# Optimization experiments

Hardware: AMD Instinct MI355X
Metric: run time of the kernel (lower is better)

Reference implementation:

```python
import jax, jax.numpy as jnp
import numpy as np

DN = ('NCDHW', 'OIDHW', 'NCDHW')
EPS = 1e-5


def conv3(x, w, b):
    y = jax.lax.conv_general_dilated(x, w, (1, 1, 1), 'SAME', dimension_numbers=DN)
    return y + b[None, :, None, None, None]


def inorm(x):
    # InstanceNorm3d, affine=False: normalize over spatial dims per (batch, channel)
    m = jnp.mean(x, axis=(2, 3, 4), keepdims=True)
    v = jnp.mean((x - m) ** 2, axis=(2, 3, 4), keepdims=True)
    return (x - m) * jax.lax.rsqrt(v + EPS)


def prelu(x, a):
    return jnp.where(x >= 0, x, a * x)


def _head(x, w1, b1, w234, b234, a, wf, bf, K):
    # 4-conv tower (conv + instancenorm + PReLU), then final conv -> (b, n_anchors_level, K)
    x = prelu(inorm(conv3(x, w1, b1)), a[0])
    for i in range(3):
        x = prelu(inorm(conv3(x, w234[i], b234[i])), a[i + 1])
    y = conv3(x, wf, bf)
    y = jnp.transpose(y, (0, 2, 3, 4, 1))  # (b, D, H, W, C)
    return y.reshape(y.shape[0], -1, K)


def setup_inputs() -> dict:
    key = jax.random.key(0)
    ks = jax.random.split(key, 32)
    IN_C, FEAT = 36, 64
    CLS_OUT = 9 * 2      # out_channels_per_pos * headers
    REG_OUT = 9 * 3 * 2  # out_channels_per_pos * dim * 2
    inp = {}
    shapes = [(1, IN_C, 32, 32, 32), (1, IN_C, 16, 16, 16), (1, IN_C, 8, 8, 8), (1, IN_C, 4, 4, 4)]
    for i, s in enumerate(shapes):
        inp[f'p{i}'] = jax.random.normal(ks[i], s, dtype=jnp.float32)
    w = lambda k, s: jax.random.normal(k, s, dtype=jnp.float32) * 0.05
    for j, h in enumerate(['cls', 'reg']):
        base = 4 + j * 10
        OUT = CLS_OUT if h == 'cls' else REG_OUT
        inp[f'{h}_w1'] = w(ks[base + 0], (FEAT, IN_C, 3, 3, 3))
        inp[f'{h}_b1'] = jnp.zeros((FEAT,), jnp.float32)
        inp[f'{h}_w234'] = w(ks[base + 1], (3, FEAT, FEAT, 3, 3, 3))
        inp[f'{h}_b234'] = jnp.zeros((3, FEAT), jnp.float32)
        inp[f'{h}_a'] = jnp.full((4,), 0.25, jnp.float32)  # PReLU init
        inp[f'{h}_wf'] = w(ks[base + 2], (OUT, FEAT, 3, 3, 3))
        inp[f'{h}_bf'] = jnp.zeros((OUT,), jnp.float32)
    return inp


def reference(p0, p1, p2, p3,
              cls_w1, cls_b1, cls_w234, cls_b234, cls_a, cls_wf, cls_bf,
              reg_w1, reg_b1, reg_w234, reg_b234, reg_a, reg_wf, reg_bf):
    feats = [p0, p1, p2, p3]
    class_logits = jnp.concatenate(
        [_head(p, cls_w1, cls_b1, cls_w234, cls_b234, cls_a, cls_wf, cls_bf, 2) for p in feats], axis=1)
    bb_outputs = jnp.concatenate(
        [_head(p, reg_w1, reg_b1, reg_w234, reg_b234, reg_a, reg_wf, reg_bf, 6) for p in feats], axis=1)
    return class_logits, bb_outputs
```

## Files before the change

kernel.cpp:

```cpp
#include <hip/hip_runtime.h>


typedef __attribute__((ext_vector_type(8)))  short short8;
typedef __attribute__((ext_vector_type(8)))  unsigned short ushort8;
typedef __attribute__((ext_vector_type(4)))  float f32x4;

static constexpr int TOTVOX    = 37440;
static constexpr int CLS_TOTAL = 673920;
static constexpr int TOTPADV   = 46352;
static constexpr size_t PAD_HSTRIDE_E = (size_t)TOTPADV * 64;
static constexpr size_t WLAYER_E = 2u * 27 * 4096;

__device__ __forceinline__ unsigned short f2b(float x) {
    unsigned int u = __float_as_uint(x);
    u += 0x7FFFu + ((u >> 16) & 1u);
    return (unsigned short)(u >> 16);
}
__device__ __forceinline__ float b2f(unsigned short h) {
    return __uint_as_float(((unsigned)h) << 16);
}

__device__ __forceinline__ int xcdswz(int orig) {
    const int xcd = orig & 7;
    return (xcd < 2 ? xcd * 147 : 294 + (xcd - 2) * 146) + (orig >> 3);
}

__device__ __forceinline__ void blkdec(int b, int& lvl, int& ls, int& S, int& P,
                                       int& loff, int& cvol, int& base)
{
    if (b < 1024)      { lvl = 0; base = b * 32; }
    else if (b < 1152) { lvl = 1; base = 32768 + (b - 1024) * 32; }
    else if (b < 1168) { lvl = 2; base = 36864 + (b - 1152) * 32; }
    else               { lvl = 3; base = 37376 + (b - 1168) * 32; }
    ls = 5 - lvl; S = 1 << ls; P = S + 2;
    loff = (lvl == 0) ? 0 : (lvl == 1) ? 32768 : (lvl == 2) ? 36864 : 37376;
    cvol = (lvl == 0) ? 0 : (lvl == 1) ? 39304 : (lvl == 2) ? 45136 : 46136;
}

__device__ __forceinline__ void voxdec(int vox, int& lvl, int& ls, int& loff,
                                       int& cvol, int& pbase)
{
    if (vox < 32768)      lvl = 0;
    else if (vox < 36864) lvl = 1;
    else if (vox < 37376) lvl = 2;
    else                  lvl = 3;
    ls = 5 - lvl;
    const int S = 1 << ls, P = S + 2;
    loff = (lvl == 0) ? 0 : (lvl == 1) ? 32768 : (lvl == 2) ? 36864 : 37376;
    cvol = (lvl == 0) ? 0 : (lvl == 1) ? 39304 : (lvl == 2) ? 45136 : 46136;
    const int v = vox - loff;
    const int x = v & (S - 1), y = (v >> ls) & (S - 1), z = v >> (2 * ls);
    pbase = ((z + 1) * P + (y + 1)) * P + (x + 1);
}

__global__ __launch_bounds__(256) void wconv_kernel(
    const float* __restrict__ cls_w1, const float* __restrict__ reg_w1,
    const float* __restrict__ cls_w234, const float* __restrict__ reg_w234,
    const float* __restrict__ cls_wf, const float* __restrict__ reg_wf,
    unsigned short* __restrict__ dst)
{
    const int id = blockIdx.x * 256 + (int)threadIdx.x;
    const int s  = id / 221184;
    const int r  = id - s * 221184;
    const int head = r / 110592;
    const int r2 = r - head * 110592;
    const int t  = r2 >> 12;
    const int q  = r2 & 4095;
    const int slice = q >> 9;
    const int co = (q >> 3) & 63;
    const int ci = slice * 8 + (q & 7);

    float val = 0.0f;
    if (s == 0) {
        if (ci < 36) {
            const float* w = head ? reg_w1 : cls_w1;
            val = w[(co * 36 + ci) * 27 + t];
        }
    } else if (s <= 3) {
        const float* w = (head ? reg_w234 : cls_w234) + (size_t)(s - 1) * 110592;
        val = w[(co * 64 + ci) * 27 + t];
    } else {
        const int OUT = head ? 54 : 18;
        if (co < OUT) {
            const float* w = head ? reg_wf : cls_wf;
            val = w[(co * 64 + ci) * 27 + t];
        }
    }
    dst[id] = f2b(val);
}

__global__ __launch_bounds__(256) void inconv_kernel(
    const float* __restrict__ p0, const float* __restrict__ p1,
    const float* __restrict__ p2, const float* __restrict__ p3,
    unsigned short* __restrict__ padin)
{
    const int id = blockIdx.x * 256 + (int)threadIdx.x;
    const int s   = id / 37440;
    const int vox = id - s * 37440;

    int lvl, ls, loff, cvol, pbase;
    voxdec(vox, lvl, ls, loff, cvol, pbase);
    const int nvox = 1 << (3 * ls);
    const int lvox = vox - loff;
    const float* src = (lvl == 0) ? p0 : (lvl == 1) ? p1 : (lvl == 2) ? p2 : p3;

    ushort8 o;
    #pragma unroll
    for (int j = 0; j < 8; ++j) {
        const int c = s * 8 + j;
        o[j] = (c < 36) ? f2b(src[c * nvox + lvox]) : (unsigned short)0;
    }
    *reinterpret_cast<ushort8*>(padin + ((size_t)s * TOTPADV + cvol + pbase) * 8) = o;
}

template<bool FINAL>
__global__ __launch_bounds__(256, 4) void conv_mfma_kernel(
    const unsigned short* __restrict__ A, const size_t a_head_stride_e,
    const unsigned short* __restrict__ W,
    const float* __restrict__ b_cls, const float* __restrict__ b_reg,
    float* __restrict__ stats, unsigned short* __restrict__ raw,
    float* __restrict__ dout)
{
    const int tid  = threadIdx.x;
    const int head = blockIdx.y;
    const int b    = xcdswz(blockIdx.x);

    int lvl, ls, S, P, loff, cvol, base;
    blkdec(b, lvl, ls, S, P, loff, cvol, base);

    const int lane = tid & 63, wv = tid >> 6;
    const int row = lane & 15, kg = lane >> 4;
    const int cout = wv * 16 + row;

    const unsigned short* Abase = A + (size_t)head * a_head_stride_e;
    const unsigned short* Wh = W + (size_t)head * (27 * 4096);

    unsigned av00, av01, av10, av11, wv0, wv1;
    {
        const int v0 = (base - loff) + row;
        const int x0 = v0 & (S - 1), y0 = (v0 >> ls) & (S - 1), z0 = v0 >> (2 * ls);
        const int pb0 = ((z0 + 1) * P + (y0 + 1)) * P + (x0 + 1);
        const int v1 = (base - loff) + 16 + row;
        const int x1 = v1 & (S - 1), y1 = (v1 >> ls) & (S - 1), z1 = v1 >> (2 * ls);
        const int pb1 = ((z1 + 1) * P + (y1 + 1)) * P + (x1 + 1);
        av00 = (unsigned)(((kg)     * TOTPADV + cvol + pb0) * 16);
        av01 = (unsigned)(((kg + 4) * TOTPADV + cvol + pb0) * 16);
        av10 = (unsigned)(((kg)     * TOTPADV + cvol + pb1) * 16);
        av11 = (unsigned)(((kg + 4) * TOTPADV + cvol + pb1) * 16);
    }
    wv0 = (unsigned)(((kg)     * 64 + cout) * 16);
    wv1 = (unsigned)(((kg + 4) * 64 + cout) * 16);

    f32x4 acc0 = {0.f,0.f,0.f,0.f}, acc1 = acc0;

    short8 a00_0,a01_0,a10_0,a11_0,w0_0,w1_0;
    short8 a00_1,a01_1,a10_1,a11_1,w0_1,w1_1;
    short8 a00_2,a01_2,a10_2,a11_2,w0_2,w1_2;

    auto ISSUE = [&](int t, short8& a00, short8& a01, short8& a10, short8& a11,
                     short8& w0, short8& w1) {
        const int dz = t / 9 - 1, dy = (t / 3) % 3 - 1, dx = t % 3 - 1;
        const unsigned short* At = Abase + (size_t)((dz * P + dy) * P + dx) * 8;
        const unsigned short* Wt = Wh + t * 4096;
        asm volatile("global_load_dwordx4 %0, %1, %2" : "=v"(a00) : "v"(av00), "s"(At));
        asm volatile("global_load_dwordx4 %0, %1, %2" : "=v"(a01) : "v"(av01), "s"(At));
        asm volatile("global_load_dwordx4 %0, %1, %2" : "=v"(a10) : "v"(av10), "s"(At));
        asm volatile("global_load_dwordx4 %0, %1, %2" : "=v"(a11) : "v"(av11), "s"(At));
        asm volatile("global_load_dwordx4 %0, %1, %2" : "=v"(w0)  : "v"(wv0),  "s"(Wt));
        asm volatile("global_load_dwordx4 %0, %1, %2" : "=v"(w1)  : "v"(wv1),  "s"(Wt));
    };
    auto CONS = [&](const short8& a00, const short8& a01, const short8& a10,
                    const short8& a11, const short8& w0, const short8& w1) {
        acc0 = __builtin_amdgcn_mfma_f32_16x16x32_bf16(a00, w0, acc0, 0, 0, 0);
        acc1 = __builtin_amdgcn_mfma_f32_16x16x32_bf16(a10, w0, acc1, 0, 0, 0);
        acc0 = __builtin_amdgcn_mfma_f32_16x16x32_bf16(a01, w1, acc0, 0, 0, 0);
        acc1 = __builtin_amdgcn_mfma_f32_16x16x32_bf16(a11, w1, acc1, 0, 0, 0);
    };

    #define SLOT0 a00_0,a01_0,a10_0,a11_0,w0_0,w1_0
    #define SLOT1 a00_1,a01_1,a10_1,a11_1,w0_1,w1_1
    #define SLOT2 a00_2,a01_2,a10_2,a11_2,w0_2,w1_2
    #define WAITV(N) do { asm volatile("s_waitcnt vmcnt(" #N ")" ::: "memory"); \
                          __builtin_amdgcn_sched_barrier(0); } while (0)

    ISSUE(0, SLOT0); ISSUE(1, SLOT1); ISSUE(2, SLOT2);
    WAITV(12); CONS(SLOT0); ISSUE(3,  SLOT0);
    WAITV(12); CONS(SLOT1); ISSUE(4,  SLOT1);
    WAITV(12); CONS(SLOT2); ISSUE(5,  SLOT2);
    WAITV(12); CONS(SLOT0); ISSUE(6,  SLOT0);
    WAITV(12); CONS(SLOT1); ISSUE(7,  SLOT1);
    WAITV(12); CONS(SLOT2); ISSUE(8,  SLOT2);
    WAITV(12); CONS(SLOT0); ISSUE(9,  SLOT0);
    WAITV(12); CONS(SLOT1); ISSUE(10, SLOT1);
    WAITV(12); CONS(SLOT2); ISSUE(11, SLOT2);
    WAITV(12); CONS(SLOT0); ISSUE(12, SLOT0);
    WAITV(12); CONS(SLOT1); ISSUE(13, SLOT1);
    WAITV(12); CONS(SLOT2); ISSUE(14, SLOT2);
    WAITV(12); CONS(SLOT0); ISSUE(15, SLOT0);
    WAITV(12); CONS(SLOT1); ISSUE(16, SLOT1);
    WAITV(12); CONS(SLOT2); ISSUE(17, SLOT2);
    WAITV(12); CONS(SLOT0); ISSUE(18, SLOT0);
    WAITV(12); CONS(SLOT1); ISSUE(19, SLOT1);
    WAITV(12); CONS(SLOT2); ISSUE(20, SLOT2);
    WAITV(12); CONS(SLOT0); ISSUE(21, SLOT0);
    WAITV(12); CONS(SLOT1); ISSUE(22, SLOT1);
    WAITV(12); CONS(SLOT2); ISSUE(23, SLOT2);
    WAITV(12); CONS(SLOT0); ISSUE(24, SLOT0);
    WAITV(12); CONS(SLOT1); ISSUE(25, SLOT1);
    WAITV(12); CONS(SLOT2); ISSUE(26, SLOT2);
    WAITV(12); CONS(SLOT0);
    WAITV(6);  CONS(SLOT1);
    WAITV(0);  CONS(SLOT2);

    #undef SLOT0
    #undef SLOT1
    #undef SLOT2
    #undef WAITV

    if constexpr (!FINAL) {
        const float bias = (head ? b_reg : b_cls)[cout];
        unsigned short* rp = raw + ((size_t)(head * 8 + (cout >> 3)) * TOTVOX) * 8
                                 + (cout & 7);
        float s1 = 0.f, s2 = 0.f;
        #pragma unroll
        for (int i = 0; i < 2; ++i) {
            const f32x4 a = i ? acc1 : acc0;
            #pragma unroll
            for (int r = 0; r < 4; ++r) {
                const float val = a[r] + bias;
                const int vg = base + i * 16 + kg * 4 + r;
                rp[(size_t)vg * 8] = f2b(val);
                s1 += val; s2 += val * val;
            }
        }
        s1 += __shfl_xor(s1, 16, 64); s1 += __shfl_xor(s1, 32, 64);
        s2 += __shfl_xor(s2, 16, 64); s2 += __shfl_xor(s2, 32, 64);
        if (lane < 16) {
            float* st = stats + ((head * 4 + lvl) * 64 + wv * 16 + lane) * 2;
            atomicAdd(st + 0, s1);
            atomicAdd(st + 1, s2);
        }
    } else {
        const int OUT = head ? 54 : 18;
        if (cout < OUT) {
            const float bias = (head ? b_reg : b_cls)[cout];
            float* ob = dout + (head ? CLS_TOTAL : 0);
            #pragma unroll
            for (int i = 0; i < 2; ++i) {
                const f32x4 a = i ? acc1 : acc0;
                #pragma unroll
                for (int r = 0; r < 4; ++r) {
                    const int vg = base + i * 16 + kg * 4 + r;
                    ob[(size_t)vg * OUT + cout] = a[r] + bias;
                }
            }
        }
    }
}

__global__ __launch_bounds__(256) void norm_kernel(
    const unsigned short* __restrict__ raw, const float* __restrict__ stats,
    const float* __restrict__ a_cls, const float* __restrict__ a_reg,
    const int layer, unsigned short* __restrict__ pad)
{
    const int tid  = threadIdx.x;
    const int head = blockIdx.y;
    const int b    = xcdswz(blockIdx.x);

    int lvl, ls, S, P, loff, cvol, base;
    blkdec(b, lvl, ls, S, P, loff, cvol, base);

    const int vg = base + (tid >> 3);
    const int v  = vg - loff;
    const int s  = tid & 7;
    const int x = v & (S - 1), y = (v >> ls) & (S - 1), z = v >> (2 * ls);
    const int pb = ((z + 1) * P + (y + 1)) * P + (x + 1);

    const float inv_n = 1.0f / (float)(1 << (3 * ls));
    const float alpha = (head ? a_reg : a_cls)[layer];
    const float* st = stats + (size_t)((head * 4 + lvl) * 64) * 2;

    const ushort8 u = *reinterpret_cast<const ushort8*>(
        raw + ((size_t)(head * 8 + s) * TOTVOX + vg) * 8);
    ushort8 o;
    #pragma unroll
    for (int j = 0; j < 8; ++j) {
        const int c = s * 8 + j;
        const float m = st[c * 2] * inv_n;
        float var = st[c * 2 + 1] * inv_n - m * m;
        const float rs = rsqrtf(fmaxf(var, 0.0f) + 1e-5f);
        float val = (b2f(u[j]) - m) * rs;
        val = (val >= 0.0f) ? val : alpha * val;
        o[j] = f2b(val);
    }
    *reinterpret_cast<ushort8*>(pad + (size_t)head * PAD_HSTRIDE_E
                                    + ((size_t)s * TOTPADV + cvol + pb) * 8) = o;
}

extern "C" void kernel_launch(void* const* d_in, const int* in_sizes, int n_in,
                              void* d_out, int out_size, void* d_ws, size_t ws_size,
                              hipStream_t stream)
{
    const float* p0      = (const float*)d_in[0];
    const float* p1      = (const float*)d_in[1];
    const float* p2      = (const float*)d_in[2];
    const float* p3      = (const float*)d_in[3];
    const float* cls_w1  = (const float*)d_in[4];
    const float* cls_b1  = (const float*)d_in[5];
    const float* cls_w234= (const float*)d_in[6];
    const float* cls_b234= (const float*)d_in[7];
    const float* cls_a   = (const float*)d_in[8];
    const float* cls_wf  = (const float*)d_in[9];
    const float* cls_bf  = (const float*)d_in[10];
    const float* reg_w1  = (const float*)d_in[11];
    const float* reg_b1  = (const float*)d_in[12];
    const float* reg_w234= (const float*)d_in[13];
    const float* reg_b234= (const float*)d_in[14];
    const float* reg_a   = (const float*)d_in[15];
    const float* reg_wf  = (const float*)d_in[16];
    const float* reg_bf  = (const float*)d_in[17];

    char* ws = (char*)d_ws;
    float*          stats  = (float*)ws;
    unsigned short* padIn0 = (unsigned short*)(ws + 16384);
    unsigned short* padA   = (unsigned short*)(ws + 5949440);
    unsigned short* padB   = (unsigned short*)(ws + 17815552);
    unsigned short* raw    = (unsigned short*)(ws + 29681664);
    unsigned short* wcvt   = (unsigned short*)(ws + 39266304);

    hipMemsetAsync(ws, 0, 29681664, stream);

    wconv_kernel<<<4320, 256, 0, stream>>>(
        cls_w1, reg_w1, cls_w234, reg_w234, cls_wf, reg_wf, wcvt);
    inconv_kernel<<<1170, 256, 0, stream>>>(p0, p1, p2, p3, padIn0);

    const dim3 cgrid(1170, 2);

    conv_mfma_kernel<false><<<cgrid, 256, 0, stream>>>(
        padIn0, 0, wcvt, cls_b1, reg_b1, stats, raw, nullptr);
    norm_kernel<<<cgrid, 256, 0, stream>>>(raw, stats, cls_a, reg_a, 0, padA);

    unsigned short* srcs[3] = { padA, padB, padA };
    unsigned short* dsts[3] = { padB, padA, padB };
    for (int l = 0; l < 3; ++l) {
        conv_mfma_kernel<false><<<cgrid, 256, 0, stream>>>(
            srcs[l], PAD_HSTRIDE_E, wcvt + (size_t)(l + 1) * WLAYER_E,
            cls_b234 + l * 64, reg_b234 + l * 64,
            stats + (l + 1) * 1024, raw, nullptr);
        norm_kernel<<<cgrid, 256, 0, stream>>>(
            raw, stats + (l + 1) * 1024, cls_a, reg_a, l + 1, dsts[l]);
    }

    conv_mfma_kernel<true><<<cgrid, 256, 0, stream>>>(
        padB, PAD_HSTRIDE_E, wcvt + 4 * WLAYER_E,
        cls_bf, reg_bf, nullptr, nullptr, (float*)d_out);
}
```

Measured before the change: 557.2 us.

## Retile conv MFMA so each wave computes all 64 output channels

Each conv block now covers 128 voxels, and each wave owns 32 voxels across all 64 output channels (4 channel groups) instead of 16 channels. Each activation fragment is loaded once per wave and reused across four weight fragments, cutting redundant activation reads from the padded buffer. The weight layout is permuted to match, the grid shrinks from 1170 to 293 blocks per head, the pipeline goes from three stages to two, and occupancy drops to 3 blocks per SIMD. The costs are more accumulator and operand registers, fewer blocks to fill the GPU, and idle waves on the smallest level.

```diff
diff --git a/kernel.cpp b/kernel.cpp
--- a/kernel.cpp
+++ b/kernel.cpp
@@ -20,13 +20,29 @@
     return __uint_as_float(((unsigned)h) << 16);
 }
 
-__device__ __forceinline__ int xcdswz(int orig) {
+__device__ __forceinline__ int xcdswz1170(int orig) {
     const int xcd = orig & 7;
     return (xcd < 2 ? xcd * 147 : 294 + (xcd - 2) * 146) + (orig >> 3);
 }
-
-__device__ __forceinline__ void blkdec(int b, int& lvl, int& ls, int& S, int& P,
-                                       int& loff, int& cvol, int& base)
+__device__ __forceinline__ int xcdswz293(int orig) {
+    const int xcd = orig & 7;
+    return (xcd < 5 ? xcd * 37 : 185 + (xcd - 5) * 36) + (orig >> 3);
+}
+
+__device__ __forceinline__ void blkdec128(int b, int& lvl, int& ls, int& S, int& P,
+                                          int& loff, int& cvol, int& base)
+{
+    if (b < 256)      { lvl = 0; base = b * 128; }
+    else if (b < 288) { lvl = 1; base = 32768 + (b - 256) * 128; }
+    else if (b < 292) { lvl = 2; base = 36864 + (b - 288) * 128; }
+    else              { lvl = 3; base = 37376; }
+    ls = 5 - lvl; S = 1 << ls; P = S + 2;
+    loff = (lvl == 0) ? 0 : (lvl == 1) ? 32768 : (lvl == 2) ? 36864 : 37376;
+    cvol = (lvl == 0) ? 0 : (lvl == 1) ? 39304 : (lvl == 2) ? 45136 : 46136;
+}
+
+__device__ __forceinline__ void blkdec32(int b, int& lvl, int& ls, int& S, int& P,
+                                         int& loff, int& cvol, int& base)
 {
     if (b < 1024)      { lvl = 0; base = b * 32; }
     else if (b < 1152) { lvl = 1; base = 32768 + (b - 1024) * 32; }
@@ -66,9 +82,10 @@
     const int r2 = r - head * 110592;
     const int t  = r2 >> 12;
     const int q  = r2 & 4095;
-    const int slice = q >> 9;
-    const int co = (q >> 3) & 63;
-    const int ci = slice * 8 + (q & 7);
+    const int kgi = q >> 10;
+    const int kb  = (q >> 9) & 1;
+    const int co  = (q >> 3) & 63;
+    const int ci  = (kb * 4 + kgi) * 8 + (q & 7);
 
     float val = 0.0f;
     if (s == 0) {
@@ -114,7 +131,7 @@
 }
 
 template<bool FINAL>
-__global__ __launch_bounds__(256, 4) void conv_mfma_kernel(
+__global__ __launch_bounds__(256, 3) void conv_mfma_kernel(
     const unsigned short* __restrict__ A, const size_t a_head_stride_e,
     const unsigned short* __restrict__ W,
     const float* __restrict__ b_cls, const float* __restrict__ b_reg,
@@ -123,135 +140,152 @@
 {
     const int tid  = threadIdx.x;
     const int head = blockIdx.y;
-    const int b    = xcdswz(blockIdx.x);
+    const int b    = xcdswz293(blockIdx.x);
 
     int lvl, ls, S, P, loff, cvol, base;
-    blkdec(b, lvl, ls, S, P, loff, cvol, base);
+    blkdec128(b, lvl, ls, S, P, loff, cvol, base);
 
     const int lane = tid & 63, wv = tid >> 6;
     const int row = lane & 15, kg = lane >> 4;
-    const int cout = wv * 16 + row;
+
+    const int wbase = base + ((lvl == 3) ? (wv & 1) : wv) * 32;
+    const bool wvalid = !(lvl == 3 && wv >= 2);
 
     const unsigned short* Abase = A + (size_t)head * a_head_stride_e;
     const unsigned short* Wh = W + (size_t)head * (27 * 4096);
 
-    unsigned av00, av01, av10, av11, wv0, wv1;
+    unsigned avF0, avF1, wvoff;
     {
-        const int v0 = (base - loff) + row;
+        const int v0 = (wbase - loff) + row;
         const int x0 = v0 & (S - 1), y0 = (v0 >> ls) & (S - 1), z0 = v0 >> (2 * ls);
         const int pb0 = ((z0 + 1) * P + (y0 + 1)) * P + (x0 + 1);
-        const int v1 = (base - loff) + 16 + row;
+        const int v1 = v0 + 16;
         const int x1 = v1 & (S - 1), y1 = (v1 >> ls) & (S - 1), z1 = v1 >> (2 * ls);
         const int pb1 = ((z1 + 1) * P + (y1 + 1)) * P + (x1 + 1);
-        av00 = (unsigned)(((kg)     * TOTPADV + cvol + pb0) * 16);
-        av01 = (unsigned)(((kg + 4) * TOTPADV + cvol + pb0) * 16);
-        av10 = (unsigned)(((kg)     * TOTPADV + cvol + pb1) * 16);
-        av11 = (unsigned)(((kg + 4) * TOTPADV + cvol + pb1) * 16);
-    }
-    wv0 = (unsigned)(((kg)     * 64 + cout) * 16);
-    wv1 = (unsigned)(((kg + 4) * 64 + cout) * 16);
-
-    f32x4 acc0 = {0.f,0.f,0.f,0.f}, acc1 = acc0;
-
-    short8 a00_0,a01_0,a10_0,a11_0,w0_0,w1_0;
-    short8 a00_1,a01_1,a10_1,a11_1,w0_1,w1_1;
-    short8 a00_2,a01_2,a10_2,a11_2,w0_2,w1_2;
-
-    auto ISSUE = [&](int t, short8& a00, short8& a01, short8& a10, short8& a11,
-                     short8& w0, short8& w1) {
+        avF0 = (unsigned)((kg * TOTPADV + cvol + pb0) * 16);
+        avF1 = (unsigned)((kg * TOTPADV + cvol + pb1) * 16);
+    }
+    wvoff = (unsigned)(kg * 2048 + row * 16);
+
+    f32x4 c[2][4];
+    #pragma unroll
+    for (int i = 0; i < 2; ++i)
+        #pragma unroll
+        for (int g = 0; g < 4; ++g) c[i][g] = f32x4{0.f, 0.f, 0.f, 0.f};
+
+    short8 aA0_0,aA1_0,aB0_0,aB1_0,w00_0,w01_0,w02_0,w03_0,w10_0,w11_0,w12_0,w13_0;
+    short8 aA0_1,aA1_1,aB0_1,aB1_1,w00_1,w01_1,w02_1,w03_1,w10_1,w11_1,w12_1,w13_1;
+
+    auto ISSUE = [&](int t,
+        short8& aA0, short8& aA1, short8& aB0, short8& aB1,
+        short8& w00, short8& w01, short8& w02, short8& w03,
+        short8& w10, short8& w11, short8& w12, short8& w13) {
         const int dz = t / 9 - 1, dy = (t / 3) % 3 - 1, dx = t % 3 - 1;
-        const unsigned short* At = Abase + (size_t)((dz * P + dy) * P + dx) * 8;
-        const unsigned short* Wt = Wh + t * 4096;
-        asm volatile("global_load_dwordx4 %0, %1, %2" : "=v"(a00) : "v"(av00), "s"(At));
-        asm volatile("global_load_dwordx4 %0, %1, %2" : "=v"(a01) : "v"(av01), "s"(At));
-        asm volatile("global_load_dwordx4 %0, %1, %2" : "=v"(a10) : "v"(av10), "s"(At));
-        asm volatile("global_load_dwordx4 %0, %1, %2" : "=v"(a11) : "v"(av11), "s"(At));
-        asm volatile("global_load_dwordx4 %0, %1, %2" : "=v"(w0)  : "v"(wv0),  "s"(Wt));
-        asm volatile("global_load_dwordx4 %0, %1, %2" : "=v"(w1)  : "v"(wv1),  "s"(Wt));
+        const unsigned short* At  = Abase + (ptrdiff_t)((dz * P + dy) * P + dx) * 8;
+        const unsigned short* At2 = At + (size_t)4 * TOTPADV * 8;
+        const unsigned short* Wt  = Wh + (size_t)t * 4096;
+        asm volatile("global_load_dwordx4 %0, %1, %2" : "=v"(aA0) : "v"(avF0), "s"(At));
+        asm volatile("global_load_dwordx4 %0, %1, %2" : "=v"(aA1) : "v"(avF0), "s"(At2));
+        asm volatile("global_load_dwordx4 %0, %1, %2" : "=v"(aB0) : "v"(avF1), "s"(At));
+        asm volatile("global_load_dwordx4 %0, %1, %2" : "=v"(aB1) : "v"(avF1), "s"(At2));
+        asm volatile("global_load_dwordx4 %0, %1, %2"             : "=v"(w00) : "v"(wvoff), "s"(Wt));
+        asm volatile("global_load_dwordx4 %0, %1, %2 offset:256"  : "=v"(w01) : "v"(wvoff), "s"(Wt));
+        asm volatile("global_load_dwordx4 %0, %1, %2 offset:512"  : "=v"(w02) : "v"(wvoff), "s"(Wt));
+        asm volatile("global_load_dwordx4 %0, %1, %2 offset:768"  : "=v"(w03) : "v"(wvoff), "s"(Wt));
+        asm volatile("global_load_dwordx4 %0, %1, %2 offset:1024" : "=v"(w10) : "v"(wvoff), "s"(Wt));
+        asm volatile("global_load_dwordx4 %0, %1, %2 offset:1280" : "=v"(w11) : "v"(wvoff), "s"(Wt));
+        asm volatile("global_load_dwordx4 %0, %1, %2 offset:1536" : "=v"(w12) : "v"(wvoff), "s"(Wt));
+        asm volatile("global_load_dwordx4 %0, %1, %2 offset:1792" : "=v"(w13) : "v"(wvoff), "s"(Wt));
     };
-    auto CONS = [&](const short8& a00, const short8& a01, const short8& a10,
-                    const short8& a11, const short8& w0, const short8& w1) {
-        acc0 = __builtin_amdgcn_mfma_f32_16x16x32_bf16(a00, w0, acc0, 0, 0, 0);
-        acc1 = __builtin_amdgcn_mfma_f32_16x16x32_bf16(a10, w0, acc1, 0, 0, 0);
-        acc0 = __builtin_amdgcn_mfma_f32_16x16x32_bf16(a01, w1, acc0, 0, 0, 0);
-        acc1 = __builtin_amdgcn_mfma_f32_16x16x32_bf16(a11, w1, acc1, 0, 0, 0);
+    auto CONS = [&](const short8& aA0, const short8& aA1,
+                    const short8& aB0, const short8& aB1,
+                    const short8& w00, const short8& w01, const short8& w02, const short8& w03,
+                    const short8& w10, const short8& w11, const short8& w12, const short8& w13) {
+        c[0][0] = __builtin_amdgcn_mfma_f32_16x16x32_bf16(aA0, w00, c[0][0], 0, 0, 0);
+        c[0][1] = __builtin_amdgcn_mfma_f32_16x16x32_bf16(aA0, w01, c[0][1], 0, 0, 0);
+        c[0][2] = __builtin_amdgcn_mfma_f32_16x16x32_bf16(aA0, w02, c[0][2], 0, 0, 0);
+        c[0][3] = __builtin_amdgcn_mfma_f32_16x16x32_bf16(aA0, w03, c[0][3], 0, 0, 0);
+        c[1][0] = __builtin_amdgcn_mfma_f32_16x16x32_bf16(aB0, w00, c[1][0], 0, 0, 0);
+        c[1][1] = __builtin_amdgcn_mfma_f32_16x16x32_bf16(aB0, w01, c[1][1], 0, 0, 0);
+        c[1][2] = __builtin_amdgcn_mfma_f32_16x16x32_bf16(aB0, w02, c[1][2], 0, 0, 0);
+        c[1][3] = __builtin_amdgcn_mfma_f32_16x16x32_bf16(aB0, w03, c[1][3], 0, 0, 0);
+        c[0][0] = __builtin_amdgcn_mfma_f32_16x16x32_bf16(aA1, w10, c[0][0], 0, 0, 0);
+        c[0][1] = __builtin_amdgcn_mfma_f32_16x16x32_bf16(aA1, w11, c[0][1], 0, 0, 0);
+        c[0][2] = __builtin_amdgcn_mfma_f32_16x16x32_bf16(aA1, w12, c[0][2], 0, 0, 0);
+        c[0][3] = __builtin_amdgcn_mfma_f32_16x16x32_bf16(aA1, w13, c[0][3], 0, 0, 0);
+        c[1][0] = __builtin_amdgcn_mfma_f32_16x16x32_bf16(aB1, w10, c[1][0], 0, 0, 0);
+        c[1][1] = __builtin_amdgcn_mfma_f32_16x16x32_bf16(aB1, w11, c[1][1], 0, 0, 0);
+        c[1][2] = __builtin_amdgcn_mfma_f32_16x16x32_bf16(aB1, w12, c[1][2], 0, 0, 0);
+        c[1][3] = __builtin_amdgcn_mfma_f32_16x16x32_bf16(aB1, w13, c[1][3], 0, 0, 0);
     };
 
-    #define SLOT0 a00_0,a01_0,a10_0,a11_0,w0_0,w1_0
-    #define SLOT1 a00_1,a01_1,a10_1,a11_1,w0_1,w1_1
-    #define SLOT2 a00_2,a01_2,a10_2,a11_2,w0_2,w1_2
+    #define SL0 aA0_0,aA1_0,aB0_0,aB1_0,w00_0,w01_0,w02_0,w03_0,w10_0,w11_0,w12_0,w13_0
+    #define SL1 aA0_1,aA1_1,aB0_1,aB1_1,w00_1,w01_1,w02_1,w03_1,w10_1,w11_1,w12_1,w13_1
     #define WAITV(N) do { asm volatile("s_waitcnt vmcnt(" #N ")" ::: "memory"); \
                           __builtin_amdgcn_sched_barrier(0); } while (0)
-
-    ISSUE(0, SLOT0); ISSUE(1, SLOT1); ISSUE(2, SLOT2);
-    WAITV(12); CONS(SLOT0); ISSUE(3,  SLOT0);
-    WAITV(12); CONS(SLOT1); ISSUE(4,  SLOT1);
-    WAITV(12); CONS(SLOT2); ISSUE(5,  SLOT2);
-    WAITV(12); CONS(SLOT0); ISSUE(6,  SLOT0);
-    WAITV(12); CONS(SLOT1); ISSUE(7,  SLOT1);
-    WAITV(12); CONS(SLOT2); ISSUE(8,  SLOT2);
-    WAITV(12); CONS(SLOT0); ISSUE(9,  SLOT0);
-    WAITV(12); CONS(SLOT1); ISSUE(10, SLOT1);
-    WAITV(12); CONS(SLOT2); ISSUE(11, SLOT2);
-    WAITV(12); CONS(SLOT0); ISSUE(12, SLOT0);
-    WAITV(12); CONS(SLOT1); ISSUE(13, SLOT1);
-    WAITV(12); CONS(SLOT2); ISSUE(14, SLOT2);
-    WAITV(12); CONS(SLOT0); ISSUE(15, SLOT0);
-    WAITV(12); CONS(SLOT1); ISSUE(16, SLOT1);
-    WAITV(12); CONS(SLOT2); ISSUE(17, SLOT2);
-    WAITV(12); CONS(SLOT0); ISSUE(18, SLOT0);
-    WAITV(12); CONS(SLOT1); ISSUE(19, SLOT1);
-    WAITV(12); CONS(SLOT2); ISSUE(20, SLOT2);
-    WAITV(12); CONS(SLOT0); ISSUE(21, SLOT0);
-    WAITV(12); CONS(SLOT1); ISSUE(22, SLOT1);
-    WAITV(12); CONS(SLOT2); ISSUE(23, SLOT2);
-    WAITV(12); CONS(SLOT0); ISSUE(24, SLOT0);
-    WAITV(12); CONS(SLOT1); ISSUE(25, SLOT1);
-    WAITV(12); CONS(SLOT2); ISSUE(26, SLOT2);
-    WAITV(12); CONS(SLOT0);
-    WAITV(6);  CONS(SLOT1);
-    WAITV(0);  CONS(SLOT2);
-
-    #undef SLOT0
-    #undef SLOT1
-    #undef SLOT2
+    #define STEP2(ta, tb) \
+        WAITV(12); CONS(SL0); ISSUE(ta, SL0); \
+        WAITV(12); CONS(SL1); ISSUE(tb, SL1);
+
+    ISSUE(0, SL0); ISSUE(1, SL1);
+    STEP2(2, 3)   STEP2(4, 5)   STEP2(6, 7)   STEP2(8, 9)
+    STEP2(10, 11) STEP2(12, 13) STEP2(14, 15) STEP2(16, 17)
+    STEP2(18, 19) STEP2(20, 21) STEP2(22, 23) STEP2(24, 25)
+    WAITV(12); CONS(SL0); ISSUE(26, SL0);
+    WAITV(12); CONS(SL1);
+    WAITV(0);  CONS(SL0);
+
+    #undef SL0
+    #undef SL1
     #undef WAITV
+    #undef STEP2
+
+    const float* bptr = head ? b_reg : b_cls;
 
     if constexpr (!FINAL) {
-        const float bias = (head ? b_reg : b_cls)[cout];
-        unsigned short* rp = raw + ((size_t)(head * 8 + (cout >> 3)) * TOTVOX) * 8
-                                 + (cout & 7);
-        float s1 = 0.f, s2 = 0.f;
-        #pragma unroll
-        for (int i = 0; i < 2; ++i) {
-            const f32x4 a = i ? acc1 : acc0;
+        if (wvalid) {
             #pragma unroll
-            for (int r = 0; r < 4; ++r) {
-                const float val = a[r] + bias;
-                const int vg = base + i * 16 + kg * 4 + r;
-                rp[(size_t)vg * 8] = f2b(val);
-                s1 += val; s2 += val * val;
+            for (int cg = 0; cg < 4; ++cg) {
+                const int cout = cg * 16 + row;
+                const float bias = bptr[cout];
+                float s1 = 0.f, s2 = 0.f;
+                #pragma unroll
+                for (int i = 0; i < 2; ++i) {
+                    #pragma unroll
+                    for (int r = 0; r < 4; ++r) {
+                        const float val = c[i][cg][r] + bias;
+                        const int vg = wbase + i * 16 + kg * 4 + r;
+                        raw[((size_t)(head * 8 + (cout >> 3)) * TOTVOX + vg) * 8
+                            + (cout & 7)] = f2b(val);
+                        s1 += val; s2 += val * val;
+                    }
+                }
+                s1 += __shfl_xor(s1, 16, 64); s1 += __shfl_xor(s1, 32, 64);
+                s2 += __shfl_xor(s2, 16, 64); s2 += __shfl_xor(s2, 32, 64);
+                if (lane < 16) {
+                    float* st = stats + ((head * 4 + lvl) * 64 + cg * 16 + lane) * 2;
+                    atomicAdd(st + 0, s1);
+                    atomicAdd(st + 1, s2);
+                }
             }
         }
-        s1 += __shfl_xor(s1, 16, 64); s1 += __shfl_xor(s1, 32, 64);
-        s2 += __shfl_xor(s2, 16, 64); s2 += __shfl_xor(s2, 32, 64);
-        if (lane < 16) {
-            float* st = stats + ((head * 4 + lvl) * 64 + wv * 16 + lane) * 2;
-            atomicAdd(st + 0, s1);
-            atomicAdd(st + 1, s2);
-        }
     } else {
-        const int OUT = head ? 54 : 18;
-        if (cout < OUT) {
-            const float bias = (head ? b_reg : b_cls)[cout];
+        if (wvalid) {
+            const int OUT = head ? 54 : 18;
             float* ob = dout + (head ? CLS_TOTAL : 0);
             #pragma unroll
-            for (int i = 0; i < 2; ++i) {
-                const f32x4 a = i ? acc1 : acc0;
-                #pragma unroll
-                for (int r = 0; r < 4; ++r) {
-                    const int vg = base + i * 16 + kg * 4 + r;
-                    ob[(size_t)vg * OUT + cout] = a[r] + bias;
+            for (int cg = 0; cg < 4; ++cg) {
+                const int cout = cg * 16 + row;
+                if (cout < OUT) {
+                    const float bias = bptr[cout];
+                    #pragma unroll
+                    for (int i = 0; i < 2; ++i) {
+                        #pragma unroll
+                        for (int r = 0; r < 4; ++r) {
+                            const int vg = wbase + i * 16 + kg * 4 + r;
+                            ob[(size_t)vg * OUT + cout] = c[i][cg][r] + bias;
+                        }
+                    }
                 }
             }
         }
@@ -265,10 +299,10 @@
 {
     const int tid  = threadIdx.x;
     const int head = blockIdx.y;
-    const int b    = xcdswz(blockIdx.x);
+    const int b    = xcdswz1170(blockIdx.x);
 
     int lvl, ls, S, P, loff, cvol, base;
-    blkdec(b, lvl, ls, S, P, loff, cvol, base);
+    blkdec32(b, lvl, ls, S, P, loff, cvol, base);
 
     const int vg = base + (tid >> 3);
     const int v  = vg - loff;
@@ -285,9 +319,9 @@
     ushort8 o;
     #pragma unroll
     for (int j = 0; j < 8; ++j) {
-        const int c = s * 8 + j;
-        const float m = st[c * 2] * inv_n;
-        float var = st[c * 2 + 1] * inv_n - m * m;
+        const int cch = s * 8 + j;
+        const float m = st[cch * 2] * inv_n;
+        float var = st[cch * 2 + 1] * inv_n - m * m;
         const float rs = rsqrtf(fmaxf(var, 0.0f) + 1e-5f);
         float val = (b2f(u[j]) - m) * rs;
         val = (val >= 0.0f) ? val : alpha * val;
@@ -334,11 +368,12 @@
         cls_w1, reg_w1, cls_w234, reg_w234, cls_wf, reg_wf, wcvt);
     inconv_kernel<<<1170, 256, 0, stream>>>(p0, p1, p2, p3, padIn0);
 
-    const dim3 cgrid(1170, 2);
+    const dim3 cgrid(293, 2);
+    const dim3 ngrid(1170, 2);
 
     conv_mfma_kernel<false><<<cgrid, 256, 0, stream>>>(
         padIn0, 0, wcvt, cls_b1, reg_b1, stats, raw, nullptr);
-    norm_kernel<<<cgrid, 256, 0, stream>>>(raw, stats, cls_a, reg_a, 0, padA);
+    norm_kernel<<<ngrid, 256, 0, stream>>>(raw, stats, cls_a, reg_a, 0, padA);
 
     unsigned short* srcs[3] = { padA, padB, padA };
     unsigned short* dsts[3] = { padB, padA, padB };
@@ -347,7 +382,7 @@
             srcs[l], PAD_HSTRIDE_E, wcvt + (size_t)(l + 1) * WLAYER_E,
             cls_b234 + l * 64, reg_b234 + l * 64,
             stats + (l + 1) * 1024, raw, nullptr);
-        norm_kernel<<<cgrid, 256, 0, stream>>>(
+        norm_kernel<<<ngrid, 256, 0, stream>>>(
             raw, stats + (l + 1) * 1024, cls_a, reg_a, l + 1, dsts[l]);
     }
 
```

After: 619.1 us. 1.11x slower.

## Stage conv tap operands through LDS with direct global-to-LDS double buffering

Applied to the files above, without the earlier changes.

The conv MFMA kernel stops loading A and W fragments per wave straight into registers with a 3-deep register pipeline. Instead, each block cooperatively copies each tap's activation and weight tile into shared memory with global_load_lds, double-buffered, and every wave then reads its fragments from LDS. This removes duplicate global loads of the same weights across waves. In exchange it adds two block barriers per tap, uses LDS, and drops the occupancy hint from launch bounds.

```diff
diff --git a/kernel.cpp b/kernel.cpp
--- a/kernel.cpp
+++ b/kernel.cpp
@@ -20,13 +20,13 @@
     return __uint_as_float(((unsigned)h) << 16);
 }
 
-__device__ __forceinline__ int xcdswz(int orig) {
+__device__ __forceinline__ int xcdswz1170(int orig) {
     const int xcd = orig & 7;
     return (xcd < 2 ? xcd * 147 : 294 + (xcd - 2) * 146) + (orig >> 3);
 }
 
-__device__ __forceinline__ void blkdec(int b, int& lvl, int& ls, int& S, int& P,
-                                       int& loff, int& cvol, int& base)
+__device__ __forceinline__ void blkdec32(int b, int& lvl, int& ls, int& S, int& P,
+                                         int& loff, int& cvol, int& base)
 {
     if (b < 1024)      { lvl = 0; base = b * 32; }
     else if (b < 1152) { lvl = 1; base = 32768 + (b - 1024) * 32; }
@@ -53,6 +53,12 @@
     pbase = ((z + 1) * P + (y + 1)) * P + (x + 1);
 }
 
+__device__ __forceinline__ void gl16(const unsigned short* g, void* l) {
+    __builtin_amdgcn_global_load_lds(
+        (const __attribute__((address_space(1))) void*)g,
+        (__attribute__((address_space(3))) void*)l, 16, 0, 0);
+}
+
 __global__ __launch_bounds__(256) void wconv_kernel(
     const float* __restrict__ cls_w1, const float* __restrict__ reg_w1,
     const float* __restrict__ cls_w234, const float* __restrict__ reg_w234,
@@ -114,19 +120,22 @@
 }
 
 template<bool FINAL>
-__global__ __launch_bounds__(256, 4) void conv_mfma_kernel(
+__global__ __launch_bounds__(256) void conv_mfma_kernel(
     const unsigned short* __restrict__ A, const size_t a_head_stride_e,
     const unsigned short* __restrict__ W,
     const float* __restrict__ b_cls, const float* __restrict__ b_reg,
     float* __restrict__ stats, unsigned short* __restrict__ raw,
     float* __restrict__ dout)
 {
+    __shared__ short8 Albuf[2][256];
+    __shared__ short8 Wlbuf[2][512];
+
     const int tid  = threadIdx.x;
     const int head = blockIdx.y;
-    const int b    = xcdswz(blockIdx.x);
+    const int b    = xcdswz1170(blockIdx.x);
 
     int lvl, ls, S, P, loff, cvol, base;
-    blkdec(b, lvl, ls, S, P, loff, cvol, base);
+    blkdec32(b, lvl, ls, S, P, loff, cvol, base);
 
     const int lane = tid & 63, wv = tid >> 6;
     const int row = lane & 15, kg = lane >> 4;
@@ -135,92 +144,66 @@
     const unsigned short* Abase = A + (size_t)head * a_head_stride_e;
     const unsigned short* Wh = W + (size_t)head * (27 * 4096);
 
-    unsigned av00, av01, av10, av11, wv0, wv1;
+    const unsigned short* aSrcBase;
     {
-        const int v0 = (base - loff) + row;
-        const int x0 = v0 & (S - 1), y0 = (v0 >> ls) & (S - 1), z0 = v0 >> (2 * ls);
-        const int pb0 = ((z0 + 1) * P + (y0 + 1)) * P + (x0 + 1);
-        const int v1 = (base - loff) + 16 + row;
-        const int x1 = v1 & (S - 1), y1 = (v1 >> ls) & (S - 1), z1 = v1 >> (2 * ls);
-        const int pb1 = ((z1 + 1) * P + (y1 + 1)) * P + (x1 + 1);
-        av00 = (unsigned)(((kg)     * TOTPADV + cvol + pb0) * 16);
-        av01 = (unsigned)(((kg + 4) * TOTPADV + cvol + pb0) * 16);
-        av10 = (unsigned)(((kg)     * TOTPADV + cvol + pb1) * 16);
-        av11 = (unsigned)(((kg + 4) * TOTPADV + cvol + pb1) * 16);
-    }
-    wv0 = (unsigned)(((kg)     * 64 + cout) * 16);
-    wv1 = (unsigned)(((kg + 4) * 64 + cout) * 16);
+        const int sl = wv * 2 + (lane >> 5);
+        const int v  = lane & 31;
+        const int iv = (base - loff) + v;
+        const int x = iv & (S - 1), y = (iv >> ls) & (S - 1), z = iv >> (2 * ls);
+        const int pb = ((z + 1) * P + (y + 1)) * P + (x + 1);
+        aSrcBase = Abase + ((size_t)sl * TOTPADV + cvol + pb) * 8;
+    }
+    const int lane8 = lane * 8;
 
     f32x4 acc0 = {0.f,0.f,0.f,0.f}, acc1 = acc0;
 
-    short8 a00_0,a01_0,a10_0,a11_0,w0_0,w1_0;
-    short8 a00_1,a01_1,a10_1,a11_1,w0_1,w1_1;
-    short8 a00_2,a01_2,a10_2,a11_2,w0_2,w1_2;
-
-    auto ISSUE = [&](int t, short8& a00, short8& a01, short8& a10, short8& a11,
-                     short8& w0, short8& w1) {
+    auto STAGE = [&](int t, int bs) {
         const int dz = t / 9 - 1, dy = (t / 3) % 3 - 1, dx = t % 3 - 1;
-        const unsigned short* At = Abase + (size_t)((dz * P + dy) * P + dx) * 8;
-        const unsigned short* Wt = Wh + t * 4096;
-        asm volatile("global_load_dwordx4 %0, %1, %2" : "=v"(a00) : "v"(av00), "s"(At));
-        asm volatile("global_load_dwordx4 %0, %1, %2" : "=v"(a01) : "v"(av01), "s"(At));
-        asm volatile("global_load_dwordx4 %0, %1, %2" : "=v"(a10) : "v"(av10), "s"(At));
-        asm volatile("global_load_dwordx4 %0, %1, %2" : "=v"(a11) : "v"(av11), "s"(At));
-        asm volatile("global_load_dwordx4 %0, %1, %2" : "=v"(w0)  : "v"(wv0),  "s"(Wt));
-        asm volatile("global_load_dwordx4 %0, %1, %2" : "=v"(w1)  : "v"(wv1),  "s"(Wt));
+        const int tapoff = ((dz * P + dy) * P + dx) * 8;
+        gl16(aSrcBase + tapoff, &Albuf[bs][wv * 64]);
+        const unsigned short* Wt = Wh + (size_t)t * 4096;
+        gl16(Wt + wv * 512 + lane8,        &Wlbuf[bs][wv * 64]);
+        gl16(Wt + 2048 + wv * 512 + lane8, &Wlbuf[bs][256 + wv * 64]);
     };
-    auto CONS = [&](const short8& a00, const short8& a01, const short8& a10,
-                    const short8& a11, const short8& w0, const short8& w1) {
+
+    #define FENCE asm volatile("" ::: "memory")
+    #define BARRIER do { FENCE; __builtin_amdgcn_s_barrier(); FENCE; } while (0)
+    #define WAITV3 do { asm volatile("s_waitcnt vmcnt(3)" ::: "memory"); \
+                        __builtin_amdgcn_sched_barrier(0); } while (0)
+    #define WAITV0 do { asm volatile("s_waitcnt vmcnt(0)" ::: "memory"); \
+                        __builtin_amdgcn_sched_barrier(0); } while (0)
+    #define LGKM0  asm volatile("s_waitcnt lgkmcnt(0)" ::: "memory")
+
+    STAGE(0, 0);
+    for (int t = 0; t < 27; ++t) {
+        const int bs = t & 1;
+        if (t < 26) { STAGE(t + 1, bs ^ 1); WAITV3; }
+        else        { WAITV0; }
+        BARRIER;
+        const short8 a00 = Albuf[bs][kg * 32 + row];
+        const short8 a10 = Albuf[bs][kg * 32 + row + 16];
+        const short8 a01 = Albuf[bs][(kg + 4) * 32 + row];
+        const short8 a11 = Albuf[bs][(kg + 4) * 32 + row + 16];
+        const short8 w0  = Wlbuf[bs][kg * 64 + cout];
+        const short8 w1  = Wlbuf[bs][256 + kg * 64 + cout];
         acc0 = __builtin_amdgcn_mfma_f32_16x16x32_bf16(a00, w0, acc0, 0, 0, 0);
         acc1 = __builtin_amdgcn_mfma_f32_16x16x32_bf16(a10, w0, acc1, 0, 0, 0);
         acc0 = __builtin_amdgcn_mfma_f32_16x16x32_bf16(a01, w1, acc0, 0, 0, 0);
         acc1 = __builtin_amdgcn_mfma_f32_16x16x32_bf16(a11, w1, acc1, 0, 0, 0);
-    };
-
-    #define SLOT0 a00_0,a01_0,a10_0,a11_0,w0_0,w1_0
-    #define SLOT1 a00_1,a01_1,a10_1,a11_1,w0_1,w1_1
-    #define SLOT2 a00_2,a01_2,a10_2,a11_2,w0_2,w1_2
-    #define WAITV(N) do { asm volatile("s_waitcnt vmcnt(" #N ")" ::: "memory"); \
-                          __builtin_amdgcn_sched_barrier(0); } while (0)
-
-    ISSUE(0, SLOT0); ISSUE(1, SLOT1); ISSUE(2, SLOT2);
-    WAITV(12); CONS(SLOT0); ISSUE(3,  SLOT0);
-    WAITV(12); CONS(SLOT1); ISSUE(4,  SLOT1);
-    WAITV(12); CONS(SLOT2); ISSUE(5,  SLOT2);
-    WAITV(12); CONS(SLOT0); ISSUE(6,  SLOT0);
-    WAITV(12); CONS(SLOT1); ISSUE(7,  SLOT1);
-    WAITV(12); CONS(SLOT2); ISSUE(8,  SLOT2);
-    WAITV(12); CONS(SLOT0); ISSUE(9,  SLOT0);
-    WAITV(12); CONS(SLOT1); ISSUE(10, SLOT1);
-    WAITV(12); CONS(SLOT2); ISSUE(11, SLOT2);
-    WAITV(12); CONS(SLOT0); ISSUE(12, SLOT0);
-    WAITV(12); CONS(SLOT1); ISSUE(13, SLOT1);
-    WAITV(12); CONS(SLOT2); ISSUE(14, SLOT2);
-    WAITV(12); CONS(SLOT0); ISSUE(15, SLOT0);
-    WAITV(12); CONS(SLOT1); ISSUE(16, SLOT1);
-    WAITV(12); CONS(SLOT2); ISSUE(17, SLOT2);
-    WAITV(12); CONS(SLOT0); ISSUE(18, SLOT0);
-    WAITV(12); CONS(SLOT1); ISSUE(19, SLOT1);
-    WAITV(12); CONS(SLOT2); ISSUE(20, SLOT2);
-    WAITV(12); CONS(SLOT0); ISSUE(21, SLOT0);
-    WAITV(12); CONS(SLOT1); ISSUE(22, SLOT1);
-    WAITV(12); CONS(SLOT2); ISSUE(23, SLOT2);
-    WAITV(12); CONS(SLOT0); ISSUE(24, SLOT0);
-    WAITV(12); CONS(SLOT1); ISSUE(25, SLOT1);
-    WAITV(12); CONS(SLOT2); ISSUE(26, SLOT2);
-    WAITV(12); CONS(SLOT0);
-    WAITV(6);  CONS(SLOT1);
-    WAITV(0);  CONS(SLOT2);
-
-    #undef SLOT0
-    #undef SLOT1
-    #undef SLOT2
-    #undef WAITV
+        LGKM0;
+        BARRIER;
+    }
+
+    #undef FENCE
+    #undef BARRIER
+    #undef WAITV3
+    #undef WAITV0
+    #undef LGKM0
+
+    const float bias = (head ? b_reg : b_cls)[cout];
 
     if constexpr (!FINAL) {
-        const float bias = (head ? b_reg : b_cls)[cout];
-        unsigned short* rp = raw + ((size_t)(head * 8 + (cout >> 3)) * TOTVOX) * 8
-                                 + (cout & 7);
+        unsigned short* rp = raw;
         float s1 = 0.f, s2 = 0.f;
         #pragma unroll
         for (int i = 0; i < 2; ++i) {
@@ -229,7 +212,8 @@
             for (int r = 0; r < 4; ++r) {
                 const float val = a[r] + bias;
                 const int vg = base + i * 16 + kg * 4 + r;
-                rp[(size_t)vg * 8] = f2b(val);
+                rp[((size_t)(head * 8 + (cout >> 3)) * TOTVOX + vg) * 8
+                   + (cout & 7)] = f2b(val);
                 s1 += val; s2 += val * val;
             }
         }
@@ -243,7 +227,6 @@
     } else {
         const int OUT = head ? 54 : 18;
         if (cout < OUT) {
-            const float bias = (head ? b_reg : b_cls)[cout];
             float* ob = dout + (head ? CLS_TOTAL : 0);
             #pragma unroll
             for (int i = 0; i < 2; ++i) {
@@ -265,10 +248,10 @@
 {
     const int tid  = threadIdx.x;
     const int head = blockIdx.y;
-    const int b    = xcdswz(blockIdx.x);
+    const int b    = xcdswz1170(blockIdx.x);
 
     int lvl, ls, S, P, loff, cvol, base;
-    blkdec(b, lvl, ls, S, P, loff, cvol, base);
+    blkdec32(b, lvl, ls, S, P, loff, cvol, base);
 
     const int vg = base + (tid >> 3);
     const int v  = vg - loff;
@@ -285,9 +268,9 @@
     ushort8 o;
     #pragma unroll
     for (int j = 0; j < 8; ++j) {
-        const int c = s * 8 + j;
-        const float m = st[c * 2] * inv_n;
-        float var = st[c * 2 + 1] * inv_n - m * m;
+        const int cch = s * 8 + j;
+        const float m = st[cch * 2] * inv_n;
+        float var = st[cch * 2 + 1] * inv_n - m * m;
         const float rs = rsqrtf(fmaxf(var, 0.0f) + 1e-5f);
         float val = (b2f(u[j]) - m) * rs;
         val = (val >= 0.0f) ? val : alpha * val;
```

Measured after the change: 526.7 us. 5.5% less time.
